# Performance work log

Measured on AMD Instinct MI355X. Metric: run time of the kernel, lower is better.

The kernel has to match this reference:

```python
import jax, jax.numpy as jnp
import numpy as np

NUM_LABELS = 512
NUM_DEMOG = 4
N = 65536
D = 512


def setup_inputs() -> dict:
    key = jax.random.key(0)
    k1, k2, k3 = jax.random.split(key, 3)
    feats = jax.random.normal(k1, (N, D), dtype=jnp.float32)
    labels = jax.random.randint(k2, (N,), 0, NUM_LABELS, dtype=jnp.int64)
    demog_labels = jax.random.randint(k3, (N,), 0, NUM_DEMOG, dtype=jnp.int64)
    return {"feats": feats, "labels": labels, "demog_labels": demog_labels}


def reference(feats, labels, demog_labels):
    # Group id = (demog, label) pair -> flat segment id.
    G = NUM_DEMOG * NUM_LABELS
    seg = (demog_labels * NUM_LABELS + labels).astype(jnp.int32)  # [N]

    ones = jnp.ones((feats.shape[0],), dtype=feats.dtype)
    cnt = jax.ops.segment_sum(ones, seg, num_segments=G)          # [G]
    sums = jax.ops.segment_sum(feats, seg, num_segments=G)        # [G, D]
    safe_cnt = jnp.maximum(cnt, 1.0)
    mu = sums / safe_cnt[:, None]                                 # per-group mean

    # Per-sample squared distance to its group mean (== diagonal of the
    # centered Gram matrix in the original, without the O(n^2) matmul).
    d = feats - mu[seg]                                           # [N, D]
    sq = jnp.sum(d * d, axis=1)                                   # [N]

    grp_mean_dist = jax.ops.segment_sum(sq, seg, num_segments=G) / safe_cnt  # [G]

    present = (cnt > 0).astype(feats.dtype).reshape(NUM_DEMOG, NUM_LABELS)
    gm = grp_mean_dist.reshape(NUM_DEMOG, NUM_LABELS)
    # Mean over present (demog, subject) groups within each demog.
    intra = jnp.sum(gm * present, axis=1) / jnp.maximum(jnp.sum(present, axis=1), 1.0)  # [NUM_DEMOG]

    mu_intra = jnp.mean(intra)
    loss = jnp.mean(jnp.abs(intra - mu_intra))
    return loss
```

## Files before the change

kernel.cpp:

```cpp
#include <hip/hip_runtime.h>
#include <hip/hip_bf16.h>

#define NN 65536
#define DD 512
#define NUM_LABELS 512
#define NUM_DEMOG 4
#define GG (NUM_DEMOG * NUM_LABELS)
#define CAP 128
#define NSLICE 2

__global__ void k_hist(const int* __restrict__ labels,
                       const int* __restrict__ demog,
                       int* __restrict__ cnt,
                       int* __restrict__ order) {
    int i = blockIdx.x * blockDim.x + threadIdx.x;
    if (i >= NN) return;
    int seg = demog[i] * NUM_LABELS + labels[i];
    int pos = atomicAdd(&cnt[seg], 1);
    if (pos < CAP) order[seg * CAP + pos] = i;
}

#define GBATCH16(BASE, IDXREG)                                                \
    {                                                                         \
        float4 v[16];                                                         \
        _Pragma("unroll")                                                     \
        for (int k = 0; k < 16; ++k) {                                        \
            int row = __shfl(IDXREG, (BASE & 63) + k);                        \
            v[k] = fv[(size_t)row * (DD / 4) + fcol];                         \
        }                                                                     \
        _Pragma("unroll")                                                     \
        for (int k = 0; k < 16; ++k) {                                        \
            float w = (BASE + k < c) ? 1.f : 0.f;                             \
            acc.x += w * v[k].x; acc.y += w * v[k].y;                         \
            acc.z += w * v[k].z; acc.w += w * v[k].w;                         \
            ssq += w * (v[k].x * v[k].x + v[k].y * v[k].y +                   \
                        v[k].z * v[k].z + v[k].w * v[k].w);                   \
        }                                                                     \
    }

__global__ __launch_bounds__(256)
void k_group(const float* __restrict__ feats,
             const int* __restrict__ cnt,
             const int* __restrict__ order,
             float* __restrict__ part) {
    int t    = threadIdx.x;
    int lane = t & 63;
    int task = blockIdx.x * 4 + (t >> 6);
    int g = task >> 1;
    int s = task & 1;

    int idx0 = order[g * CAP + lane];
    int idx1 = order[g * CAP + 64 + lane];
    int c = cnt[g];
    if (c > CAP) c = CAP;
    idx0 = (lane < c) ? idx0 : 0;
    idx1 = (64 + lane < c) ? idx1 : 0;

    const float4* fv = (const float4*)feats;
    int fcol = s * 64 + lane;

    float4 acc = make_float4(0.f, 0.f, 0.f, 0.f);
    float ssq = 0.f;

    GBATCH16(0, idx0)
    if (c > 16) GBATCH16(16, idx0)
    if (c > 32) GBATCH16(32, idx0)
    if (c > 48) GBATCH16(48, idx0)
    for (int j = 64; j < c; ++j) {
        int row = __shfl(idx1, j - 64);
        float4 v = fv[(size_t)row * (DD / 4) + fcol];
        acc.x += v.x; acc.y += v.y; acc.z += v.z; acc.w += v.w;
        ssq += v.x * v.x + v.y * v.y + v.z * v.z + v.w * v.w;
    }

    float n2p = acc.x * acc.x + acc.y * acc.y + acc.z * acc.z + acc.w * acc.w;
    for (int off = 32; off > 0; off >>= 1) {
        ssq += __shfl_down(ssq, off);
        n2p += __shfl_down(n2p, off);
    }
    if (lane == 0) {
        float val = 0.f;
        if (c > 0) val = ssq - n2p / (float)c;
        part[task] = val;
    }
}

__global__ __launch_bounds__(256)
void k_final(const int* __restrict__ cnt,
             const float* __restrict__ part,
             float* __restrict__ out) {
    int t = threadIdx.x;
    __shared__ float sred[8];
    __shared__ float intra[NUM_DEMOG];

    for (int d = 0; d < NUM_DEMOG; ++d) {
        float s = 0.f;
        float p = 0.f;
        for (int l = t; l < NUM_LABELS; l += 256) {
            int g = d * NUM_LABELS + l;
            int c = cnt[g];
            if (c > 0) {
                float q = part[2 * g] + part[2 * g + 1];
                s += q / (float)c;
                p += 1.f;
            }
        }
        for (int off = 32; off > 0; off >>= 1) {
            s += __shfl_down(s, off);
            p += __shfl_down(p, off);
        }
        if ((t & 63) == 0) {
            int wid = t >> 6;
            sred[wid * 2]     = s;
            sred[wid * 2 + 1] = p;
        }
        __syncthreads();
        if (t == 0) {
            float S = sred[0] + sred[2] + sred[4] + sred[6];
            float P = sred[1] + sred[3] + sred[5] + sred[7];
            intra[d] = S / fmaxf(P, 1.f);
        }
        __syncthreads();
    }
    if (t == 0) {
        float m = 0.f;
        for (int d = 0; d < NUM_DEMOG; ++d) m += intra[d];
        m *= (1.f / NUM_DEMOG);
        float l = 0.f;
        for (int d = 0; d < NUM_DEMOG; ++d) l += fabsf(intra[d] - m);
        out[0] = l * (1.f / NUM_DEMOG);
    }
}

extern "C" void kernel_launch(void* const* d_in, const int* in_sizes, int n_in,
                              void* d_out, int out_size, void* d_ws, size_t ws_size,
                              hipStream_t stream) {
    const float* feats = (const float*)d_in[0];
    const int* labels  = (const int*)d_in[1];
    const int* demog   = (const int*)d_in[2];
    float* out = (float*)d_out;

    int*   cnt   = (int*)d_ws;
    float* part  = (float*)(cnt + GG);
    int*   order = (int*)(part + GG * NSLICE);

    hipMemsetAsync(d_ws, 0, GG * sizeof(int), stream);

    k_hist<<<NN / 256, 256, 0, stream>>>(labels, demog, cnt, order);
    k_group<<<GG * NSLICE / 4, 256, 0, stream>>>(feats, cnt, order, part);
    k_final<<<1, 256, 0, stream>>>(cnt, part, out);
}
```

Baseline: 214.4 us.

## Split each group across 8 column slices with 4 row groups per wave

Each wave now covers 16 float4 columns (256 bytes) of a group, and its four 16-lane row groups read different rows at the same time. Partial column sums are combined with xor shuffles, and the duplicated n2p is corrected with a 0.25 factor. This raises the number of waves from 4096 to 16384 and halves the batch register array, aiming for more memory-level parallelism and occupancy. In exchange, each row read becomes a 256-byte segment instead of 1 KB, and there are extra shuffle reductions.

```diff
diff --git a/kernel.cpp b/kernel.cpp
--- a/kernel.cpp
+++ b/kernel.cpp
@@ -7,7 +7,7 @@
 #define NUM_DEMOG 4
 #define GG (NUM_DEMOG * NUM_LABELS)
 #define CAP 128
-#define NSLICE 2
+#define NSLICE 8
 
 __global__ void k_hist(const int* __restrict__ labels,
                        const int* __restrict__ demog,
@@ -20,17 +20,17 @@
     if (pos < CAP) order[seg * CAP + pos] = i;
 }
 
-#define GBATCH16(BASE, IDXREG)                                                \
+#define GBATCH8(BASE, IDXREG)                                                 \
     {                                                                         \
-        float4 v[16];                                                         \
+        float4 v[8];                                                          \
         _Pragma("unroll")                                                     \
-        for (int k = 0; k < 16; ++k) {                                        \
-            int row = __shfl(IDXREG, (BASE & 63) + k);                        \
+        for (int k = 0; k < 8; ++k) {                                         \
+            int row = __shfl(IDXREG, ((BASE)&63) + 4 * k + rgrp);             \
             v[k] = fv[(size_t)row * (DD / 4) + fcol];                         \
         }                                                                     \
         _Pragma("unroll")                                                     \
-        for (int k = 0; k < 16; ++k) {                                        \
-            float w = (BASE + k < c) ? 1.f : 0.f;                             \
+        for (int k = 0; k < 8; ++k) {                                         \
+            float w = ((BASE) + 4 * k + rgrp < c) ? 1.f : 0.f;                \
             acc.x += w * v[k].x; acc.y += w * v[k].y;                         \
             acc.z += w * v[k].z; acc.w += w * v[k].w;                         \
             ssq += w * (v[k].x * v[k].x + v[k].y * v[k].y +                   \
@@ -46,8 +46,10 @@
     int t    = threadIdx.x;
     int lane = t & 63;
     int task = blockIdx.x * 4 + (t >> 6);
-    int g = task >> 1;
-    int s = task & 1;
+    int g = task >> 3;
+    int s = task & 7;
+    int rgrp = lane >> 4;
+    int tcol = lane & 15;
 
     int idx0 = order[g * CAP + lane];
     int idx1 = order[g * CAP + 64 + lane];
@@ -57,30 +59,37 @@
     idx1 = (64 + lane < c) ? idx1 : 0;
 
     const float4* fv = (const float4*)feats;
-    int fcol = s * 64 + lane;
+    int fcol = s * 16 + tcol;
 
     float4 acc = make_float4(0.f, 0.f, 0.f, 0.f);
     float ssq = 0.f;
 
-    GBATCH16(0, idx0)
-    if (c > 16) GBATCH16(16, idx0)
-    if (c > 32) GBATCH16(32, idx0)
-    if (c > 48) GBATCH16(48, idx0)
-    for (int j = 64; j < c; ++j) {
+    GBATCH8(0, idx0)
+    if (c > 32) GBATCH8(32, idx0)
+    for (int j = 64 + rgrp; j < c; j += 4) {
         int row = __shfl(idx1, j - 64);
         float4 v = fv[(size_t)row * (DD / 4) + fcol];
         acc.x += v.x; acc.y += v.y; acc.z += v.z; acc.w += v.w;
         ssq += v.x * v.x + v.y * v.y + v.z * v.z + v.w * v.w;
     }
 
+    acc.x += __shfl(acc.x, lane ^ 16);
+    acc.y += __shfl(acc.y, lane ^ 16);
+    acc.z += __shfl(acc.z, lane ^ 16);
+    acc.w += __shfl(acc.w, lane ^ 16);
+    acc.x += __shfl(acc.x, lane ^ 32);
+    acc.y += __shfl(acc.y, lane ^ 32);
+    acc.z += __shfl(acc.z, lane ^ 32);
+    acc.w += __shfl(acc.w, lane ^ 32);
     float n2p = acc.x * acc.x + acc.y * acc.y + acc.z * acc.z + acc.w * acc.w;
+
     for (int off = 32; off > 0; off >>= 1) {
         ssq += __shfl_down(ssq, off);
         n2p += __shfl_down(n2p, off);
     }
     if (lane == 0) {
         float val = 0.f;
-        if (c > 0) val = ssq - n2p / (float)c;
+        if (c > 0) val = ssq - 0.25f * n2p / (float)c;
         part[task] = val;
     }
 }
@@ -100,7 +109,9 @@
             int g = d * NUM_LABELS + l;
             int c = cnt[g];
             if (c > 0) {
-                float q = part[2 * g] + part[2 * g + 1];
+                float q = 0.f;
+#pragma unroll
+                for (int k = 0; k < NSLICE; ++k) q += part[NSLICE * g + k];
                 s += q / (float)c;
                 p += 1.f;
             }
```

Measured after the change: 212.8 us. About the same (-0.7%).
